# Performance work log

Measured on AMD Instinct MI355X. Metric: run time of the kernel, lower is better.

Reference implementation:

```python
import jax, jax.numpy as jnp
import numpy as np

B, S, D, H = 4, 2048, 1024, 16
HD = D // H
DFF = 4 * D
NUM_LAYERS = 12
RES = 1.0 / float(np.sqrt(NUM_LAYERS))
SCALE = 1.0 / float(np.sqrt(D))  # module divides by sqrt(embed_dim), not head_dim
EPS = 1e-5


def setup_inputs() -> dict:
    key = jax.random.key(0)
    ks = jax.random.split(key, 12)
    s = 0.02
    p = lambda k, shp: (jax.random.normal(k, shp, jnp.float32) * s)
    return {
        "x": jax.random.normal(ks[0], (B, S, D), jnp.float32),
        "Wq": p(ks[1], (D, D)), "bq": jnp.zeros((D,), jnp.float32),
        "Wk": p(ks[2], (D, D)), "bk": jnp.zeros((D,), jnp.float32),
        "Wv": p(ks[3], (D, D)), "bv": jnp.zeros((D,), jnp.float32),
        "Wo": p(ks[4], (D, D)), "bo": jnp.zeros((D,), jnp.float32),
        "g1": jnp.ones((D,), jnp.float32), "be1": jnp.zeros((D,), jnp.float32),
        "g2": jnp.ones((D,), jnp.float32), "be2": jnp.zeros((D,), jnp.float32),
        "W1": p(ks[5], (D, DFF)), "b1": jnp.zeros((DFF,), jnp.float32),
        "W2": p(ks[6], (DFF, D)), "b2": jnp.zeros((D,), jnp.float32),
    }


def _layernorm(x, g, b):
    m = jnp.mean(x, axis=-1, keepdims=True)
    v = jnp.mean((x - m) ** 2, axis=-1, keepdims=True)
    return (x - m) * jax.lax.rsqrt(v + EPS) * g + b


def _attention(x, Wq, bq, Wk, bk, Wv, bv, Wo, bo):
    b, s, d = x.shape
    q = (x @ Wq + bq).reshape(b, s, H, HD)
    k = (x @ Wk + bk).reshape(b, s, H, HD)
    v = (x @ Wv + bv).reshape(b, s, H, HD)
    scores = jnp.einsum('bqhd,bkhd->bhqk', q, k) * SCALE  # [B,H,S,S]
    mask = jnp.tril(jnp.ones((s, s), dtype=bool))
    scores = jnp.where(mask, scores, -jnp.inf)
    attn = jax.nn.softmax(scores, axis=-1)  # dropout_rate=0 -> identity
    out = jnp.einsum('bhqk,bkhd->bqhd', attn, v).reshape(b, s, d)
    return out @ Wo + bo


def reference(x, Wq, bq, Wk, bk, Wv, bv, Wo, bo, g1, be1, g2, be2, W1, b1, W2, b2):
    x = x + RES * _attention(_layernorm(x, g1, be1), Wq, bq, Wk, bk, Wv, bv, Wo, bo)
    h = _layernorm(x, g2, be2)
    ffn = jax.nn.relu(h @ W1 + b1) @ W2 + b2
    x = x + RES * ffn
    return x
```

## Files before the change

### kernel.cpp

```cpp
#include <hip/hip_runtime.h>

typedef unsigned short ushort_t;
typedef unsigned int uint32;
typedef __attribute__((ext_vector_type(4))) float f32x4;
typedef __attribute__((ext_vector_type(8))) short bf16x8;

#define B_   4
#define S_   2048
#define D_   1024
#define H_   16
#define HD_  64
#define DFF_ 4096
#define M_   (B_ * S_)

#define RES_   0.28867513459481287f
#define SCALE_ 0.03125f
#define EPS_   1e-5f
#define LOG2E_ 1.4426950408889634f

__device__ __forceinline__ ushort_t f2bf(float f) {
    union { float f; uint32 u; } c; c.f = f;
    uint32 u = c.u + 0x7fffu + ((c.u >> 16) & 1u);
    return (ushort_t)(u >> 16);
}
__device__ __forceinline__ float bf2f(ushort_t h) {
    union { uint32 u; float f; } c; c.u = ((uint32)h) << 16;
    return c.f;
}
__device__ __forceinline__ float fexp2(float x) {
    float r; asm("v_exp_f32 %0, %1" : "=v"(r) : "v"(x)); return r;
}
__device__ __forceinline__ uint32 cvt_pk_bf16(float lo, float hi) {
    uint32 r;
    asm("v_cvt_pk_bf16_f32 %0, %1, %2" : "=v"(r) : "v"(lo), "v"(hi));
    return r;
}

__global__ __launch_bounds__(256) void transpose_cast_kernel(
    const float* __restrict__ W, ushort_t* __restrict__ Wt, int K, int N)
{
    __shared__ float tile[32][33];
    const int bx = blockIdx.x * 32;
    const int by = blockIdx.y * 32;
    const int tx = threadIdx.x;
    const int ty = threadIdx.y;
    #pragma unroll
    for (int i = 0; i < 32; i += 8)
        tile[ty + i][tx] = W[(size_t)(by + ty + i) * N + bx + tx];
    __syncthreads();
    #pragma unroll
    for (int i = 0; i < 32; i += 8)
        Wt[(size_t)(bx + ty + i) * K + by + tx] = f2bf(tile[tx][ty + i]);
}

__global__ void concat_bias_kernel(const float* __restrict__ bq,
                                   const float* __restrict__ bk,
                                   const float* __restrict__ bv,
                                   float* __restrict__ bqkv)
{
    int i = blockIdx.x * blockDim.x + threadIdx.x;
    if (i < 3 * D_) {
        float v = (i < D_) ? bq[i] : (i < 2 * D_) ? bk[i - D_] : bv[i - 2 * D_];
        bqkv[i] = v;
    }
}

__global__ __launch_bounds__(256) void ln_kernel(
    const float* __restrict__ x, const float* __restrict__ g,
    const float* __restrict__ be, ushort_t* __restrict__ out)
{
    const int row = blockIdx.x;
    const int t = threadIdx.x;
    const int lane = t & 63;
    const int wave = t >> 6;
    const float4* xr = (const float4*)(x + (size_t)row * D_);
    float4 v = xr[t];
    float s  = v.x + v.y + v.z + v.w;
    float s2 = v.x * v.x + v.y * v.y + v.z * v.z + v.w * v.w;
    #pragma unroll
    for (int off = 32; off; off >>= 1) {
        s  += __shfl_xor(s, off);
        s2 += __shfl_xor(s2, off);
    }
    __shared__ float red[8];
    if (lane == 0) { red[wave * 2] = s; red[wave * 2 + 1] = s2; }
    __syncthreads();
    s  = red[0] + red[2] + red[4] + red[6];
    s2 = red[1] + red[3] + red[5] + red[7];
    const float mean = s * (1.0f / D_);
    const float var  = s2 * (1.0f / D_) - mean * mean;
    const float rstd = rsqrtf(var + EPS_);
    const float4 gv  = ((const float4*)g)[t];
    const float4 bv  = ((const float4*)be)[t];
    ushort_t o[4];
    o[0] = f2bf((v.x - mean) * rstd * gv.x + bv.x);
    o[1] = f2bf((v.y - mean) * rstd * gv.y + bv.y);
    o[2] = f2bf((v.z - mean) * rstd * gv.z + bv.z);
    o[3] = f2bf((v.w - mean) * rstd * gv.w + bv.w);
    *(ushort2*)&out[(size_t)row * D_ + t * 4]     = make_ushort2(o[0], o[1]);
    *(ushort2*)&out[(size_t)row * D_ + t * 4 + 2] = make_ushort2(o[2], o[3]);
}

template <int MODE>
__global__ __launch_bounds__(512, 2) void gemm_bt2_kernel(
    const ushort_t* __restrict__ A, const ushort_t* __restrict__ Bt,
    const float* __restrict__ bias, const float* __restrict__ res,
    void* __restrict__ Cout, int M, int N, int K, int gx)
{
    __shared__ __align__(16) ushort_t As[2][256 * 32];
    __shared__ __align__(16) ushort_t Bs[2][128 * 32];

    const int tid  = threadIdx.x;
    const int w    = tid >> 6;
    const int lane = tid & 63;
    const int l15  = lane & 15;
    const int g    = lane >> 4;

    const int cpx = gridDim.x >> 3;
    const int swz = (blockIdx.x & 7) * cpx + (blockIdx.x >> 3);
    const int bx = swz % gx, by = swz / gx;
    const int m0 = by * 256, n0 = bx * 128;

    const int wm = (w >> 1) * 64;
    const int wn = (w & 1) * 64;

    const int La0 = w * 64 + lane;
    const int La1 = 512 + La0;
    const int Lb  = w * 64 + lane;
    const int rowA0 = La0 >> 2, cA0 = (La0 & 3) ^ (rowA0 & 3);
    const int rowA1 = La1 >> 2, cA1 = (La1 & 3) ^ (rowA1 & 3);
    const int rowB  = Lb  >> 2, cB  = (Lb  & 3) ^ (rowB  & 3);
    const ushort_t* srcA0 = A  + (size_t)(m0 + rowA0) * K + cA0 * 8;
    const ushort_t* srcA1 = A  + (size_t)(m0 + rowA1) * K + cA1 * 8;
    const ushort_t* srcB  = Bt + (size_t)(n0 + rowB)  * K + cB  * 8;
    const int ldsA0 = (w * 64) * 8;
    const int ldsA1 = (512 + w * 64) * 8;
    const int ldsB  = (w * 64) * 8;

    #define STAGE(t_, p_)                                                         \
        do {                                                                      \
            __builtin_amdgcn_global_load_lds(                                     \
                (const __attribute__((address_space(1))) void*)(srcA0 + (t_) * 32), \
                (__attribute__((address_space(3))) void*)(&As[p_][ldsA0]), 16, 0, 0); \
            __builtin_amdgcn_global_load_lds(                                     \
                (const __attribute__((address_space(1))) void*)(srcA1 + (t_) * 32), \
                (__attribute__((address_space(3))) void*)(&As[p_][ldsA1]), 16, 0, 0); \
            __builtin_amdgcn_global_load_lds(                                     \
                (const __attribute__((address_space(1))) void*)(srcB + (t_) * 32),  \
                (__attribute__((address_space(3))) void*)(&Bs[p_][ldsB]), 16, 0, 0);  \
        } while (0)

    f32x4 acc[4][4] = {};
    const int NT = K >> 5;

    STAGE(0, 0);
    __syncthreads();

    for (int t = 0; t < NT; ++t) {
        const int cur = t & 1;
        if (t + 1 < NT) STAGE(t + 1, cur ^ 1);

        bf16x8 af[4], bfr[4];
        #pragma unroll
        for (int mf = 0; mf < 4; ++mf) {
            const int row = wm + mf * 16 + l15;
            const int cs  = g ^ (row & 3);
            af[mf] = *(const bf16x8*)&As[cur][row * 32 + cs * 8];
        }
        #pragma unroll
        for (int nf = 0; nf < 4; ++nf) {
            const int row = wn + nf * 16 + l15;
            const int cs  = g ^ (row & 3);
            bfr[nf] = *(const bf16x8*)&Bs[cur][row * 32 + cs * 8];
        }
        __builtin_amdgcn_s_setprio(1);
        #pragma unroll
        for (int mf = 0; mf < 4; ++mf)
            #pragma unroll
            for (int nf = 0; nf < 4; ++nf)
                acc[mf][nf] = __builtin_amdgcn_mfma_f32_16x16x32_bf16(
                    af[mf], bfr[nf], acc[mf][nf], 0, 0, 0);
        __builtin_amdgcn_s_setprio(0);
        __syncthreads();
    }
    #undef STAGE

    const int rbase = g * 4;
    #pragma unroll
    for (int mf = 0; mf < 4; ++mf) {
        #pragma unroll
        for (int nf = 0; nf < 4; ++nf) {
            const int col = n0 + wn + nf * 16 + l15;
            const float bcol = bias[col];
            #pragma unroll
            for (int r = 0; r < 4; ++r) {
                const int row = m0 + wm + mf * 16 + rbase + r;
                float v = acc[mf][nf][r] + bcol;
                const size_t idx = (size_t)row * N + col;
                if (MODE == 0) {
                    ((ushort_t*)Cout)[idx] = f2bf(v);
                } else if (MODE == 1) {
                    ((ushort_t*)Cout)[idx] = f2bf(fmaxf(v, 0.0f));
                } else {
                    ((float*)Cout)[idx] = res[idx] + RES_ * v;
                }
            }
        }
    }
}

__global__ __launch_bounds__(256) void fattn_kernel(
    const ushort_t* __restrict__ qkv, ushort_t* __restrict__ out)
{
    __shared__ __align__(16) ushort_t Ks[64 * 64];
    __shared__ __align__(16) ushort_t Vt[64 * 64];
    __shared__ __align__(16) ushort_t Ps[4][16 * 64];

    const int tid  = threadIdx.x;
    const int lane = tid & 63;
    const int w    = tid >> 6;
    const int bh = blockIdx.y;
    const int b = bh >> 4, h = bh & 15;

    const int l15 = lane & 15;
    const int g   = lane >> 4;

    const size_t rs = 3 * D_;
    const ushort_t* Qg = qkv + (size_t)b * S_ * rs + h * HD_;
    const ushort_t* Kg = Qg + D_;

    const int skey = tid >> 3;
    const int sc   = tid & 7;

    #pragma unroll
    for (int half = 0; half < 2; ++half) {
        const int qt = half ? blockIdx.x : (S_ / 64 - 1) - blockIdx.x;
        const int q0 = qt * 64;
        const int nkb = qt + 1;

        bf16x8 qf[2];
        {
            const int qrow = q0 + w * 16 + l15;
            #pragma unroll
            for (int kk = 0; kk < 2; ++kk) {
                bf16x8 tq = *(const bf16x8*)(Qg + (size_t)qrow * rs + kk * 32 + g * 8);
                #pragma unroll
                for (int e = 0; e < 8; ++e)
                    tq[e] = (short)f2bf(bf2f((ushort_t)tq[e]) * (SCALE_ * LOG2E_));
                qf[kk] = tq;
            }
        }

        float mrow = -1e30f, lrow = 0.f;
        f32x4 oacc[4] = {};

        bf16x8 kvreg[2], vvreg[2];
        #pragma unroll
        for (int pass = 0; pass < 2; ++pass) {
            const ushort_t* src = Kg + (size_t)(pass * 32 + skey) * rs + sc * 8;
            kvreg[pass] = *(const bf16x8*)src;
            vvreg[pass] = *(const bf16x8*)(src + D_);
        }

        for (int kb = 0; kb < nkb; ++kb) {
            __syncthreads();
            #pragma unroll
            for (int pass = 0; pass < 2; ++pass) {
                const int key = pass * 32 + skey;
                *(bf16x8*)&Ks[key * 64 + ((sc ^ (key & 7)) << 3)] = kvreg[pass];
                #pragma unroll
                for (int j = 0; j < 8; ++j) {
                    const int d  = sc * 8 + j;
                    const int cp = (key >> 3) ^ (d & 7) ^ ((d >> 3) & 7);
                    Vt[d * 64 + (cp << 3) + (key & 7)] = (ushort_t)vvreg[pass][j];
                }
            }
            if (kb + 1 < nkb) {
                #pragma unroll
                for (int pass = 0; pass < 2; ++pass) {
                    const ushort_t* src =
                        Kg + (size_t)((kb + 1) * 64 + pass * 32 + skey) * rs + sc * 8;
                    kvreg[pass] = *(const bf16x8*)src;
                    vvreg[pass] = *(const bf16x8*)(src + D_);
                }
            }
            __syncthreads();

            f32x4 sf[4] = {};
            __builtin_amdgcn_s_setprio(1);
            #pragma unroll
            for (int kk = 0; kk < 2; ++kk) {
                const int cc = kk * 4 + g;
                #pragma unroll
                for (int nf = 0; nf < 4; ++nf) {
                    const int keyr = nf * 16 + l15;
                    bf16x8 kf = *(const bf16x8*)&Ks[keyr * 64 + ((cc ^ (keyr & 7)) << 3)];
                    sf[nf] = __builtin_amdgcn_mfma_f32_16x16x32_bf16(kf, qf[kk], sf[nf], 0, 0, 0);
                }
            }
            __builtin_amdgcn_s_setprio(0);

            if (kb == nkb - 1) {
                const int q = q0 + w * 16 + l15;
                #pragma unroll
                for (int nf = 0; nf < 4; ++nf)
                    #pragma unroll
                    for (int r = 0; r < 4; ++r)
                        if (kb * 64 + nf * 16 + g * 4 + r > q) sf[nf][r] = -1e30f;
            }
            float mx = -1e30f;
            #pragma unroll
            for (int nf = 0; nf < 4; ++nf)
                #pragma unroll
                for (int r = 0; r < 4; ++r) mx = fmaxf(mx, sf[nf][r]);
            mx = fmaxf(mx, __shfl_xor(mx, 16));
            mx = fmaxf(mx, __shfl_xor(mx, 32));

            if (!__all(mx - mrow <= 8.0f)) {
                const float mnew = fmaxf(mrow, mx);
                const float corr = fexp2(mrow - mnew);
                mrow = mnew;
                lrow *= corr;
                #pragma unroll
                for (int r = 0; r < 4; ++r) {
                    const float cr = __shfl(corr, g * 4 + r, 16);
                    #pragma unroll
                    for (int nf = 0; nf < 4; ++nf) oacc[nf][r] *= cr;
                }
            }

            {
                const int qrow = l15;
                float psum = 0.f;
                #pragma unroll
                for (int nf = 0; nf < 4; ++nf) {
                    const float p0 = fexp2(sf[nf][0] - mrow);
                    const float p1 = fexp2(sf[nf][1] - mrow);
                    const float p2 = fexp2(sf[nf][2] - mrow);
                    const float p3 = fexp2(sf[nf][3] - mrow);
                    psum += (p0 + p1) + (p2 + p3);
                    uint2 pk = make_uint2(cvt_pk_bf16(p0, p1), cvt_pk_bf16(p2, p3));
                    const int c16 = ((nf << 1) + (g >> 1)) ^ (qrow & 7);
                    *(uint2*)((char*)Ps[w] + qrow * 128 + c16 * 16 + (g & 1) * 8) = pk;
                }
                psum += __shfl_xor(psum, 16);
                psum += __shfl_xor(psum, 32);
                lrow += psum;
            }

            #pragma unroll
            for (int kk = 0; kk < 2; ++kk) {
                const int cc = kk * 4 + g;
                const int qrow = l15;
                const int c16 = cc ^ (qrow & 7);
                bf16x8 pa = *(const bf16x8*)((const char*)Ps[w] + qrow * 128 + c16 * 16);
                __builtin_amdgcn_s_setprio(1);
                #pragma unroll
                for (int nf = 0; nf < 4; ++nf) {
                    const int dr  = nf * 16 + l15;
                    const int cvp = cc ^ (dr & 7) ^ ((dr >> 3) & 7);
                    bf16x8 vf = *(const bf16x8*)&Vt[dr * 64 + (cvp << 3)];
                    oacc[nf] = __builtin_amdgcn_mfma_f32_16x16x32_bf16(pa, vf, oacc[nf], 0, 0, 0);
                }
                __builtin_amdgcn_s_setprio(0);
            }
        }

        const float linv = 1.0f / lrow;
        #pragma unroll
        for (int r = 0; r < 4; ++r) {
            const float li = __shfl(linv, g * 4 + r, 16);
            const int q = q0 + w * 16 + g * 4 + r;
            ushort_t* op = out + (size_t)(b * S_ + q) * D_ + h * HD_;
            #pragma unroll
            for (int nf = 0; nf < 4; ++nf)
                op[nf * 16 + l15] = f2bf(oacc[nf][r] * li);
        }
    }
}

extern "C" void kernel_launch(void* const* d_in, const int* in_sizes, int n_in,
                              void* d_out, int out_size, void* d_ws, size_t ws_size,
                              hipStream_t stream)
{
    const float* x   = (const float*)d_in[0];
    const float* Wq  = (const float*)d_in[1];
    const float* bq  = (const float*)d_in[2];
    const float* Wk  = (const float*)d_in[3];
    const float* bk  = (const float*)d_in[4];
    const float* Wv  = (const float*)d_in[5];
    const float* bv  = (const float*)d_in[6];
    const float* Wo  = (const float*)d_in[7];
    const float* bo  = (const float*)d_in[8];
    const float* g1  = (const float*)d_in[9];
    const float* be1 = (const float*)d_in[10];
    const float* g2  = (const float*)d_in[11];
    const float* be2 = (const float*)d_in[12];
    const float* W1  = (const float*)d_in[13];
    const float* b1  = (const float*)d_in[14];
    const float* W2  = (const float*)d_in[15];
    const float* b2  = (const float*)d_in[16];
    float* out = (float*)d_out;

    char* ws = (char*)d_ws;
    size_t o = 0;
    auto alloc = [&](size_t bytes) { size_t r = o; o = (o + bytes + 255) & ~(size_t)255; return r; };
    ushort_t* Wqkvt = (ushort_t*)(ws + alloc((size_t)3 * D_ * D_ * 2));
    ushort_t* Wot   = (ushort_t*)(ws + alloc((size_t)D_ * D_ * 2));
    ushort_t* W1t   = (ushort_t*)(ws + alloc((size_t)DFF_ * D_ * 2));
    ushort_t* W2t   = (ushort_t*)(ws + alloc((size_t)D_ * DFF_ * 2));
    float*    bqkv  = (float*)(ws + alloc((size_t)3 * D_ * 4));
    ushort_t* lnbuf = (ushort_t*)(ws + alloc((size_t)M_ * D_ * 2));
    ushort_t* bigbuf= (ushort_t*)(ws + alloc((size_t)M_ * DFF_ * 2));
    ushort_t* attnb = (ushort_t*)(ws + alloc((size_t)M_ * D_ * 2));
    float*    x1    = (float*)(ws + alloc((size_t)M_ * D_ * 4));

    dim3 tblock(32, 8);
    transpose_cast_kernel<<<dim3(D_/32, D_/32), tblock, 0, stream>>>(Wq, Wqkvt,            D_, D_);
    transpose_cast_kernel<<<dim3(D_/32, D_/32), tblock, 0, stream>>>(Wk, Wqkvt + D_*D_,    D_, D_);
    transpose_cast_kernel<<<dim3(D_/32, D_/32), tblock, 0, stream>>>(Wv, Wqkvt + 2*D_*D_,  D_, D_);
    transpose_cast_kernel<<<dim3(D_/32, D_/32), tblock, 0, stream>>>(Wo, Wot,              D_, D_);
    transpose_cast_kernel<<<dim3(DFF_/32, D_/32), tblock, 0, stream>>>(W1, W1t,            D_, DFF_);
    transpose_cast_kernel<<<dim3(D_/32, DFF_/32), tblock, 0, stream>>>(W2, W2t,            DFF_, D_);
    concat_bias_kernel<<<12, 256, 0, stream>>>(bq, bk, bv, bqkv);

    ln_kernel<<<M_, 256, 0, stream>>>(x, g1, be1, lnbuf);
    gemm_bt2_kernel<0><<<(M_/256)*(3*D_/128), 512, 0, stream>>>(
        lnbuf, Wqkvt, bqkv, nullptr, bigbuf, M_, 3*D_, D_, 3*D_/128);
    fattn_kernel<<<dim3(S_/128, B_*H_), 256, 0, stream>>>(bigbuf, attnb);
    gemm_bt2_kernel<2><<<(M_/256)*(D_/128), 512, 0, stream>>>(
        attnb, Wot, bo, x, x1, M_, D_, D_, D_/128);
    ln_kernel<<<M_, 256, 0, stream>>>(x1, g2, be2, lnbuf);
    gemm_bt2_kernel<1><<<(M_/256)*(DFF_/128), 512, 0, stream>>>(
        lnbuf, W1t, b1, nullptr, bigbuf, M_, DFF_, D_, DFF_/128);
    gemm_bt2_kernel<2><<<(M_/256)*(D_/128), 512, 0, stream>>>(
        bigbuf, W2t, b2, x1, out, M_, D_, DFF_, D_/128);
}
```

Measured before the change: 416.4 us.

## Triple-buffer GEMM LDS pipeline and use 128-row tiles for N=1024 GEMMs

The GEMM kernel moves from a double-buffered LDS pipeline to a three-stage ring that prefetches two K-tiles ahead. It replaces __syncthreads with an explicit vmcnt wait plus s_barrier so loads can stay in flight across iterations. The XOR swizzle on LDS reads and writes is removed. The N=1024 GEMMs (output projection and FFN down) now use 128x128 tiles with 256 threads to double their block count. This trades more LDS per block and possible bank conflicts from the dropped swizzle for better latency hiding and occupancy on the narrow GEMMs.

```diff
diff --git a/kernel.cpp b/kernel.cpp
--- a/kernel.cpp
+++ b/kernel.cpp
@@ -101,14 +101,20 @@
     *(ushort2*)&out[(size_t)row * D_ + t * 4 + 2] = make_ushort2(o[2], o[3]);
 }
 
-template <int MODE>
-__global__ __launch_bounds__(512, 2) void gemm_bt2_kernel(
+template <int MODE, int BM>
+__global__ __launch_bounds__((BM == 256) ? 512 : 256, (BM == 256) ? 2 : 3)
+void gemm_bt3_kernel(
     const ushort_t* __restrict__ A, const ushort_t* __restrict__ Bt,
     const float* __restrict__ bias, const float* __restrict__ res,
     void* __restrict__ Cout, int M, int N, int K, int gx)
 {
-    __shared__ __align__(16) ushort_t As[2][256 * 32];
-    __shared__ __align__(16) ushort_t Bs[2][128 * 32];
+    constexpr int THREADS = (BM == 256) ? 512 : 256;
+    constexpr int APASS = (BM * 4) / THREADS;
+    constexpr int BPASS = (128 * 4) / THREADS;
+    constexpr int LOADS = APASS + BPASS;
+
+    __shared__ __align__(16) ushort_t As[3][BM * 32];
+    __shared__ __align__(16) ushort_t Bs[3][128 * 32];
 
     const int tid  = threadIdx.x;
     const int w    = tid >> 6;
@@ -119,60 +125,62 @@
     const int cpx = gridDim.x >> 3;
     const int swz = (blockIdx.x & 7) * cpx + (blockIdx.x >> 3);
     const int bx = swz % gx, by = swz / gx;
-    const int m0 = by * 256, n0 = bx * 128;
+    const int m0 = by * BM, n0 = bx * 128;
 
     const int wm = (w >> 1) * 64;
     const int wn = (w & 1) * 64;
 
-    const int La0 = w * 64 + lane;
-    const int La1 = 512 + La0;
-    const int Lb  = w * 64 + lane;
-    const int rowA0 = La0 >> 2, cA0 = (La0 & 3) ^ (rowA0 & 3);
-    const int rowA1 = La1 >> 2, cA1 = (La1 & 3) ^ (rowA1 & 3);
-    const int rowB  = Lb  >> 2, cB  = (Lb  & 3) ^ (rowB  & 3);
-    const ushort_t* srcA0 = A  + (size_t)(m0 + rowA0) * K + cA0 * 8;
-    const ushort_t* srcA1 = A  + (size_t)(m0 + rowA1) * K + cA1 * 8;
-    const ushort_t* srcB  = Bt + (size_t)(n0 + rowB)  * K + cB  * 8;
-    const int ldsA0 = (w * 64) * 8;
-    const int ldsA1 = (512 + w * 64) * 8;
-    const int ldsB  = (w * 64) * 8;
-
-    #define STAGE(t_, p_)                                                         \
-        do {                                                                      \
-            __builtin_amdgcn_global_load_lds(                                     \
-                (const __attribute__((address_space(1))) void*)(srcA0 + (t_) * 32), \
-                (__attribute__((address_space(3))) void*)(&As[p_][ldsA0]), 16, 0, 0); \
-            __builtin_amdgcn_global_load_lds(                                     \
-                (const __attribute__((address_space(1))) void*)(srcA1 + (t_) * 32), \
-                (__attribute__((address_space(3))) void*)(&As[p_][ldsA1]), 16, 0, 0); \
-            __builtin_amdgcn_global_load_lds(                                     \
-                (const __attribute__((address_space(1))) void*)(srcB + (t_) * 32),  \
-                (__attribute__((address_space(3))) void*)(&Bs[p_][ldsB]), 16, 0, 0);  \
+    const ushort_t* srcA[APASS];
+    const ushort_t* srcB[BPASS];
+    int ldsA[APASS], ldsB[BPASS];
+    #pragma unroll
+    for (int p = 0; p < APASS; ++p) {
+        const int L = p * THREADS + tid;
+        srcA[p] = A + (size_t)(m0 + (L >> 2)) * K + (L & 3) * 8;
+        ldsA[p] = (p * THREADS + w * 64) * 8;
+    }
+    #pragma unroll
+    for (int p = 0; p < BPASS; ++p) {
+        const int L = p * THREADS + tid;
+        srcB[p] = Bt + (size_t)(n0 + (L >> 2)) * K + (L & 3) * 8;
+        ldsB[p] = (p * THREADS + w * 64) * 8;
+    }
+
+    #define STAGE(t_, buf_)                                                        \
+        do {                                                                       \
+            _Pragma("unroll")                                                      \
+            for (int p = 0; p < APASS; ++p)                                        \
+                __builtin_amdgcn_global_load_lds(                                  \
+                    (const __attribute__((address_space(1))) void*)(srcA[p] + (t_) * 32), \
+                    (__attribute__((address_space(3))) void*)(&As[buf_][ldsA[p]]), 16, 0, 0); \
+            _Pragma("unroll")                                                      \
+            for (int p = 0; p < BPASS; ++p)                                        \
+                __builtin_amdgcn_global_load_lds(                                  \
+                    (const __attribute__((address_space(1))) void*)(srcB[p] + (t_) * 32), \
+                    (__attribute__((address_space(3))) void*)(&Bs[buf_][ldsB[p]]), 16, 0, 0); \
         } while (0)
 
     f32x4 acc[4][4] = {};
     const int NT = K >> 5;
 
     STAGE(0, 0);
-    __syncthreads();
+    STAGE(1, 1);
+    asm volatile("s_waitcnt vmcnt(%0)" :: "n"(LOADS) : "memory");
+    __builtin_amdgcn_s_barrier();
 
     for (int t = 0; t < NT; ++t) {
-        const int cur = t & 1;
-        if (t + 1 < NT) STAGE(t + 1, cur ^ 1);
+        const int cur = t % 3;
+        const bool more = (t + 2 < NT);
+        if (more) STAGE(t + 2, (t + 2) % 3);
 
         bf16x8 af[4], bfr[4];
         #pragma unroll
-        for (int mf = 0; mf < 4; ++mf) {
-            const int row = wm + mf * 16 + l15;
-            const int cs  = g ^ (row & 3);
-            af[mf] = *(const bf16x8*)&As[cur][row * 32 + cs * 8];
-        }
-        #pragma unroll
-        for (int nf = 0; nf < 4; ++nf) {
-            const int row = wn + nf * 16 + l15;
-            const int cs  = g ^ (row & 3);
-            bfr[nf] = *(const bf16x8*)&Bs[cur][row * 32 + cs * 8];
-        }
+        for (int mf = 0; mf < 4; ++mf)
+            af[mf] = *(const bf16x8*)&As[cur][(wm + mf * 16 + l15) * 32 + g * 8];
+        #pragma unroll
+        for (int nf = 0; nf < 4; ++nf)
+            bfr[nf] = *(const bf16x8*)&Bs[cur][(wn + nf * 16 + l15) * 32 + g * 8];
+
         __builtin_amdgcn_s_setprio(1);
         #pragma unroll
         for (int mf = 0; mf < 4; ++mf)
@@ -181,7 +189,12 @@
                 acc[mf][nf] = __builtin_amdgcn_mfma_f32_16x16x32_bf16(
                     af[mf], bfr[nf], acc[mf][nf], 0, 0, 0);
         __builtin_amdgcn_s_setprio(0);
-        __syncthreads();
+
+        if (more)
+            asm volatile("s_waitcnt vmcnt(%0)" :: "n"(LOADS) : "memory");
+        else
+            asm volatile("s_waitcnt vmcnt(0)" ::: "memory");
+        __builtin_amdgcn_s_barrier();
     }
     #undef STAGE
 
@@ -425,14 +438,14 @@
     concat_bias_kernel<<<12, 256, 0, stream>>>(bq, bk, bv, bqkv);
 
     ln_kernel<<<M_, 256, 0, stream>>>(x, g1, be1, lnbuf);
-    gemm_bt2_kernel<0><<<(M_/256)*(3*D_/128), 512, 0, stream>>>(
+    gemm_bt3_kernel<0, 256><<<(M_/256)*(3*D_/128), 512, 0, stream>>>(
         lnbuf, Wqkvt, bqkv, nullptr, bigbuf, M_, 3*D_, D_, 3*D_/128);
     fattn_kernel<<<dim3(S_/128, B_*H_), 256, 0, stream>>>(bigbuf, attnb);
-    gemm_bt2_kernel<2><<<(M_/256)*(D_/128), 512, 0, stream>>>(
+    gemm_bt3_kernel<2, 128><<<(M_/128)*(D_/128), 256, 0, stream>>>(
         attnb, Wot, bo, x, x1, M_, D_, D_, D_/128);
     ln_kernel<<<M_, 256, 0, stream>>>(x1, g2, be2, lnbuf);
-    gemm_bt2_kernel<1><<<(M_/256)*(DFF_/128), 512, 0, stream>>>(
+    gemm_bt3_kernel<1, 256><<<(M_/256)*(DFF_/128), 512, 0, stream>>>(
         lnbuf, W1t, b1, nullptr, bigbuf, M_, DFF_, D_, DFF_/128);
-    gemm_bt2_kernel<2><<<(M_/256)*(D_/128), 512, 0, stream>>>(
+    gemm_bt3_kernel<2, 128><<<(M_/128)*(D_/128), 256, 0, stream>>>(
         bigbuf, W2t, b2, x1, out, M_, D_, DFF_, D_/128);
 }
```

Result: no change. 410.7 us (-1.4%).

## Rework GEMM mainloop into triple-buffered BK=64 pipeline with interleaved loads

Applied to the files above, without the earlier changes.

The bf16 GEMM kernel now uses a K-tile of 64 with three LDS buffers and prefetches two tiles ahead. Global-to-LDS copies are interleaved with the MFMA phases, separated by explicit barriers and a vmcnt wait in place of a full syncthreads per tile. The LDS swizzle is widened to 8 chunks to match the wider rows. The aim is to hide global load latency and cut per-tile synchronisation overhead. The cost is larger LDS use (about 144KB), which drops occupancy to one block per CU, and correctness now depends on the manual wait counts.

```diff
diff --git a/kernel.cpp b/kernel.cpp
--- a/kernel.cpp
+++ b/kernel.cpp
@@ -35,6 +35,11 @@
     asm("v_cvt_pk_bf16_f32 %0, %1, %2" : "=v"(r) : "v"(lo), "v"(hi));
     return r;
 }
+
+#define GLDS(src_, dst_)                                                     \
+    __builtin_amdgcn_global_load_lds(                                        \
+        (const __attribute__((address_space(1))) void*)(src_),               \
+        (__attribute__((address_space(3))) void*)(dst_), 16, 0, 0)
 
 __global__ __launch_bounds__(256) void transpose_cast_kernel(
     const float* __restrict__ W, ushort_t* __restrict__ Wt, int K, int N)
@@ -102,19 +107,20 @@
 }
 
 template <int MODE>
-__global__ __launch_bounds__(512, 2) void gemm_bt2_kernel(
+__global__ __launch_bounds__(512, 1) void gemm8_kernel(
     const ushort_t* __restrict__ A, const ushort_t* __restrict__ Bt,
     const float* __restrict__ bias, const float* __restrict__ res,
     void* __restrict__ Cout, int M, int N, int K, int gx)
 {
-    __shared__ __align__(16) ushort_t As[2][256 * 32];
-    __shared__ __align__(16) ushort_t Bs[2][128 * 32];
+    __shared__ __align__(16) ushort_t As[3][256 * 64];
+    __shared__ __align__(16) ushort_t Bs[3][128 * 64];
 
     const int tid  = threadIdx.x;
     const int w    = tid >> 6;
     const int lane = tid & 63;
     const int l15  = lane & 15;
     const int g    = lane >> 4;
+    const int rp   = l15 & 7;
 
     const int cpx = gridDim.x >> 3;
     const int swz = (blockIdx.x & 7) * cpx + (blockIdx.x >> 3);
@@ -124,66 +130,106 @@
     const int wm = (w >> 1) * 64;
     const int wn = (w & 1) * 64;
 
-    const int La0 = w * 64 + lane;
-    const int La1 = 512 + La0;
-    const int Lb  = w * 64 + lane;
-    const int rowA0 = La0 >> 2, cA0 = (La0 & 3) ^ (rowA0 & 3);
-    const int rowA1 = La1 >> 2, cA1 = (La1 & 3) ^ (rowA1 & 3);
-    const int rowB  = Lb  >> 2, cB  = (Lb  & 3) ^ (rowB  & 3);
-    const ushort_t* srcA0 = A  + (size_t)(m0 + rowA0) * K + cA0 * 8;
-    const ushort_t* srcA1 = A  + (size_t)(m0 + rowA1) * K + cA1 * 8;
-    const ushort_t* srcB  = Bt + (size_t)(n0 + rowB)  * K + cB  * 8;
-    const int ldsA0 = (w * 64) * 8;
-    const int ldsA1 = (512 + w * 64) * 8;
-    const int ldsB  = (w * 64) * 8;
-
-    #define STAGE(t_, p_)                                                         \
-        do {                                                                      \
-            __builtin_amdgcn_global_load_lds(                                     \
-                (const __attribute__((address_space(1))) void*)(srcA0 + (t_) * 32), \
-                (__attribute__((address_space(3))) void*)(&As[p_][ldsA0]), 16, 0, 0); \
-            __builtin_amdgcn_global_load_lds(                                     \
-                (const __attribute__((address_space(1))) void*)(srcA1 + (t_) * 32), \
-                (__attribute__((address_space(3))) void*)(&As[p_][ldsA1]), 16, 0, 0); \
-            __builtin_amdgcn_global_load_lds(                                     \
-                (const __attribute__((address_space(1))) void*)(srcB + (t_) * 32),  \
-                (__attribute__((address_space(3))) void*)(&Bs[p_][ldsB]), 16, 0, 0);  \
+    const ushort_t* srcA[4];
+    const ushort_t* srcB[2];
+    int ldsA[4], ldsB[2];
+    #pragma unroll
+    for (int p = 0; p < 4; ++p) {
+        const int L = p * 512 + tid;
+        const int row = L >> 3;
+        srcA[p] = A + (size_t)(m0 + row) * K + (((L & 7) ^ (row & 7)) << 3);
+        ldsA[p] = (p * 512 + w * 64) * 8;
+    }
+    #pragma unroll
+    for (int p = 0; p < 2; ++p) {
+        const int L = p * 512 + tid;
+        const int row = L >> 3;
+        srcB[p] = Bt + (size_t)(n0 + row) * K + (((L & 7) ^ (row & 7)) << 3);
+        ldsB[p] = (p * 512 + w * 64) * 8;
+    }
+
+    #define LDA(mf_, kk_)  (*(const bf16x8*)&Ac[(wm + (mf_) * 16 + l15) * 64 + \
+                              ((((kk_) * 4 + g) ^ rp) << 3)])
+    #define LDB(nf_, kk_)  (*(const bf16x8*)&Bc[(wn + (nf_) * 16 + l15) * 64 + \
+                              ((((kk_) * 4 + g) ^ rp) << 3)])
+    #define MM_PAIR(mfb_)                                                      \
+        do {                                                                   \
+            _Pragma("unroll")                                                  \
+            for (int nf = 0; nf < 4; ++nf) {                                   \
+                acc[(mfb_)][nf] = __builtin_amdgcn_mfma_f32_16x16x32_bf16(     \
+                    a0, bb[nf], acc[(mfb_)][nf], 0, 0, 0);                     \
+                acc[(mfb_) + 1][nf] = __builtin_amdgcn_mfma_f32_16x16x32_bf16( \
+                    a1, bb[nf], acc[(mfb_) + 1][nf], 0, 0, 0);                 \
+            }                                                                  \
         } while (0)
 
     f32x4 acc[4][4] = {};
-    const int NT = K >> 5;
-
-    STAGE(0, 0);
-    __syncthreads();
+    const int NT = K >> 6;
+
+    #pragma unroll
+    for (int p = 0; p < 4; ++p) GLDS(srcA[p], &As[0][ldsA[p]]);
+    #pragma unroll
+    for (int p = 0; p < 2; ++p) GLDS(srcB[p], &Bs[0][ldsB[p]]);
+    #pragma unroll
+    for (int p = 0; p < 4; ++p) GLDS(srcA[p] + 64, &As[1][ldsA[p]]);
+    #pragma unroll
+    for (int p = 0; p < 2; ++p) GLDS(srcB[p] + 64, &Bs[1][ldsB[p]]);
+    asm volatile("s_waitcnt vmcnt(6)" ::: "memory");
+    __builtin_amdgcn_s_barrier();
 
     for (int t = 0; t < NT; ++t) {
-        const int cur = t & 1;
-        if (t + 1 < NT) STAGE(t + 1, cur ^ 1);
-
-        bf16x8 af[4], bfr[4];
+        const int cur = t % 3;
+        const int nb  = (t + 2) % 3;
+        const bool st = (t + 2 < NT);
+        const size_t koff = (size_t)(t + 2) * 64;
+        const ushort_t* __restrict__ Ac = &As[cur][0];
+        const ushort_t* __restrict__ Bc = &Bs[cur][0];
+
+        bf16x8 bb[4], a0, a1;
+
         #pragma unroll
-        for (int mf = 0; mf < 4; ++mf) {
-            const int row = wm + mf * 16 + l15;
-            const int cs  = g ^ (row & 3);
-            af[mf] = *(const bf16x8*)&As[cur][row * 32 + cs * 8];
-        }
+        for (int nf = 0; nf < 4; ++nf) bb[nf] = LDB(nf, 0);
+        a0 = LDA(0, 0); a1 = LDA(1, 0);
+        if (st) { GLDS(srcA[0] + koff, &As[nb][ldsA[0]]);
+                  GLDS(srcA[1] + koff, &As[nb][ldsA[1]]); }
+        __builtin_amdgcn_s_barrier();
+        __builtin_amdgcn_s_setprio(1);
+        MM_PAIR(0);
+        __builtin_amdgcn_s_setprio(0);
+        __builtin_amdgcn_s_barrier();
+
+        a0 = LDA(2, 0); a1 = LDA(3, 0);
+        if (st) { GLDS(srcA[2] + koff, &As[nb][ldsA[2]]);
+                  GLDS(srcA[3] + koff, &As[nb][ldsA[3]]); }
+        __builtin_amdgcn_s_barrier();
+        __builtin_amdgcn_s_setprio(1);
+        MM_PAIR(2);
+        __builtin_amdgcn_s_setprio(0);
+        __builtin_amdgcn_s_barrier();
+
         #pragma unroll
-        for (int nf = 0; nf < 4; ++nf) {
-            const int row = wn + nf * 16 + l15;
-            const int cs  = g ^ (row & 3);
-            bfr[nf] = *(const bf16x8*)&Bs[cur][row * 32 + cs * 8];
-        }
+        for (int nf = 0; nf < 4; ++nf) bb[nf] = LDB(nf, 1);
+        a0 = LDA(0, 1); a1 = LDA(1, 1);
+        if (st) { GLDS(srcB[0] + koff, &Bs[nb][ldsB[0]]);
+                  GLDS(srcB[1] + koff, &Bs[nb][ldsB[1]]); }
+        __builtin_amdgcn_s_barrier();
         __builtin_amdgcn_s_setprio(1);
-        #pragma unroll
-        for (int mf = 0; mf < 4; ++mf)
-            #pragma unroll
-            for (int nf = 0; nf < 4; ++nf)
-                acc[mf][nf] = __builtin_amdgcn_mfma_f32_16x16x32_bf16(
-                    af[mf], bfr[nf], acc[mf][nf], 0, 0, 0);
+        MM_PAIR(0);
         __builtin_amdgcn_s_setprio(0);
-        __syncthreads();
-    }
-    #undef STAGE
+        __builtin_amdgcn_s_barrier();
+
+        a0 = LDA(2, 1); a1 = LDA(3, 1);
+        __builtin_amdgcn_s_barrier();
+        __builtin_amdgcn_s_setprio(1);
+        MM_PAIR(2);
+        __builtin_amdgcn_s_setprio(0);
+        if (st) asm volatile("s_waitcnt vmcnt(6)" ::: "memory");
+        else    asm volatile("s_waitcnt vmcnt(0)" ::: "memory");
+        __builtin_amdgcn_s_barrier();
+    }
+    #undef LDA
+    #undef LDB
+    #undef MM_PAIR
 
     const int rbase = g * 4;
     #pragma unroll
@@ -425,14 +471,14 @@
     concat_bias_kernel<<<12, 256, 0, stream>>>(bq, bk, bv, bqkv);
 
     ln_kernel<<<M_, 256, 0, stream>>>(x, g1, be1, lnbuf);
-    gemm_bt2_kernel<0><<<(M_/256)*(3*D_/128), 512, 0, stream>>>(
+    gemm8_kernel<0><<<(M_/256)*(3*D_/128), 512, 0, stream>>>(
         lnbuf, Wqkvt, bqkv, nullptr, bigbuf, M_, 3*D_, D_, 3*D_/128);
     fattn_kernel<<<dim3(S_/128, B_*H_), 256, 0, stream>>>(bigbuf, attnb);
-    gemm_bt2_kernel<2><<<(M_/256)*(D_/128), 512, 0, stream>>>(
+    gemm8_kernel<2><<<(M_/256)*(D_/128), 512, 0, stream>>>(
         attnb, Wot, bo, x, x1, M_, D_, D_, D_/128);
     ln_kernel<<<M_, 256, 0, stream>>>(x1, g2, be2, lnbuf);
-    gemm_bt2_kernel<1><<<(M_/256)*(DFF_/128), 512, 0, stream>>>(
+    gemm8_kernel<1><<<(M_/256)*(DFF_/128), 512, 0, stream>>>(
         lnbuf, W1t, b1, nullptr, bigbuf, M_, DFF_, D_, DFF_/128);
-    gemm_bt2_kernel<2><<<(M_/256)*(D_/128), 512, 0, stream>>>(
+    gemm8_kernel<2><<<(M_/256)*(D_/128), 512, 0, stream>>>(
         bigbuf, W2t, b2, x1, out, M_, D_, DFF_, D_/128);
 }
```

New measurement: 429.3 us. +3.1%, slower.
